# Optimization experiments

Hardware: AMD Instinct MI355X
Metric: run time of the kernel (lower is better)

The kernel has to match this reference:

```python
import jax, jax.numpy as jnp
import numpy as np

B, S, D, NL, H, KV, F, V, R = 4, 1024, 2048, 2, 16, 4, 8192, 32000, 16
HD = D // H                      # 128, Llama-3 head dim
LORA_SCALE = 32.0 / 16.0         # alpha / r
ROPE_THETA = 500000.0
EPS = 1e-5


def _rope_tables(seq_len, hd):
    inv = 1.0 / (ROPE_THETA ** (jnp.arange(0, hd, 2, dtype=jnp.float32) / hd))
    freqs = jnp.arange(seq_len, dtype=jnp.float32)[:, None] * inv[None, :]   # [S, hd/2]
    emb = jnp.concatenate([freqs, freqs], axis=-1)                           # [S, hd]
    return jnp.cos(emb), jnp.sin(emb)


def _apply_rope(x, cos, sin):
    # x: [B, S, nh, HD]; LLaMA rotate_half convention
    h = x.shape[-1] // 2
    rot = jnp.concatenate([-x[..., h:], x[..., :h]], axis=-1)
    return x * cos[None, :, None, :] + rot * sin[None, :, None, :]


def _rmsnorm(x, w):
    return x * jax.lax.rsqrt(jnp.mean(x * x, axis=-1, keepdims=True) + EPS) * w


def _forward(embed, wq, wk, wv, wo, laq, lbq, lav, lbv, wg, wu, wd, n1, n2, nf,
             input_ids, attention_mask):
    b, s = input_ids.shape
    cos, sin = _rope_tables(s, HD)
    amask = attention_mask.astype(bool)
    # causal AND key-padding mask: [B, 1, S, S]
    mask = jnp.tril(jnp.ones((s, s), bool))[None, None] & amask[:, None, None, :]
    x = embed[input_ids]                                   # [B, S, D]
    for l in range(NL):
        h = _rmsnorm(x, n1[l])
        # base projection + LoRA adapter (q and v only, as in target_modules)
        q = h @ wq[l] + ((h @ laq[l].T) @ lbq[l].T) * LORA_SCALE
        k = h @ wk[l]
        v = h @ wv[l] + ((h @ lav[l].T) @ lbv[l].T) * LORA_SCALE
        q = _apply_rope(q.reshape(b, s, H, HD), cos, sin)
        k = _apply_rope(k.reshape(b, s, KV, HD), cos, sin)
        v = v.reshape(b, s, KV, HD)
        k = jnp.repeat(k, H // KV, axis=2)                 # GQA expand
        v = jnp.repeat(v, H // KV, axis=2)
        scores = jnp.einsum('bqhd,bkhd->bhqk', q, k) / jnp.float32(np.sqrt(HD))
        scores = jnp.where(mask, scores, jnp.float32(-1e9))
        attn = jax.nn.softmax(scores, axis=-1)
        o = jnp.einsum('bhqk,bkhd->bqhd', attn, v).reshape(b, s, D)
        x = x + o @ wo[l]
        h2 = _rmsnorm(x, n2[l])
        x = x + (jax.nn.silu(h2 @ wg[l]) * (h2 @ wu[l])) @ wd[l]
    h = _rmsnorm(x, nf)                                    # final norm -> last_hidden_state
    m = attention_mask.astype(jnp.float32)[..., None]
    return (h * m).sum(axis=1) / jnp.clip(m.sum(axis=1), 1e-9)   # masked mean pool [B, D]


def setup_inputs() -> dict:
    key = jax.random.key(0)
    ks = jax.random.split(key, 14)
    sd = 0.02
    nrm = lambda k, shape: sd * jax.random.normal(k, shape, dtype=jnp.float32)
    return {
        'embed': nrm(ks[0], (V, D)),
        'wq': nrm(ks[1], (NL, D, D)),
        'wk': nrm(ks[2], (NL, D, KV * HD)),
        'wv': nrm(ks[3], (NL, D, KV * HD)),
        'wo': nrm(ks[4], (NL, D, D)),
        'laq': nrm(ks[5], (NL, R, D)),
        'lbq': nrm(ks[6], (NL, D, R)),
        'lav': nrm(ks[7], (NL, R, D)),
        'lbv': nrm(ks[8], (NL, KV * HD, R)),
        'wg': nrm(ks[9], (NL, D, F)),
        'wu': nrm(ks[10], (NL, D, F)),
        'wd': nrm(ks[11], (NL, F, D)),
        'n1': jnp.ones((NL, D), jnp.float32),
        'n2': jnp.ones((NL, D), jnp.float32),
        'nf': jnp.ones((D,), jnp.float32),
        'input_ids': jax.random.randint(ks[12], (B, S), 0, V, dtype=jnp.int32),
        'attention_mask': jnp.ones((B, S), jnp.int32),
    }


def reference(embed, wq, wk, wv, wo, laq, lbq, lav, lbv, wg, wu, wd, n1, n2, nf,
              input_ids, attention_mask):
    return _forward(embed, wq, wk, wv, wo, laq, lbq, lav, lbv, wg, wu, wd,
                    n1, n2, nf, input_ids, attention_mask)
```

## Files before the change

kernel.cpp:

```cpp
#include <hip/hip_runtime.h>
#include <math.h>

#define B_  4
#define S_  1024
#define D_  2048
#define NL_ 2
#define H_  16
#define KV_ 4
#define F_  8192
#define R_  16
#define HD_ 128
#define BS_ (B_*S_)
#define QT2 32
#define KBLK 64
#define NQKV 3072

typedef unsigned short u16;
typedef __attribute__((ext_vector_type(8))) __bf16 bf16x8;
typedef __attribute__((ext_vector_type(4))) float  f32x4;

__device__ __forceinline__ u16 f2bf(float f) {
    unsigned x = __float_as_uint(f);
    unsigned r = (x + 0x7fffu + ((x >> 16) & 1u)) >> 16;
    return (u16)r;
}
__device__ __forceinline__ float bf2f(u16 u) {
    return __uint_as_float(((unsigned)u) << 16);
}

__device__ __forceinline__ void gload16(const void* g, void* l) {
    __builtin_amdgcn_global_load_lds((const __attribute__((address_space(1))) void*)g,
                                     (__attribute__((address_space(3))) void*)l, 16, 0, 0);
}

__global__ void embed_kernel(const float* __restrict__ embed,
                             const int* __restrict__ ids,
                             float* __restrict__ x) {
    int tok = blockIdx.x;
    int id  = ids[tok];
    const float4* src = (const float4*)(embed + (size_t)id * D_);
    float4*       dst = (float4*)(x + (size_t)tok * D_);
    for (int i = threadIdx.x; i < D_/4; i += blockDim.x) dst[i] = src[i];
}

template<int OUTBF>
__global__ __launch_bounds__(256) void rmsnorm_kernel(const float* __restrict__ x,
                                                      const float* __restrict__ w,
                                                      void* __restrict__ out) {
    int row = blockIdx.x;
    const float4* xr = (const float4*)(x + (size_t)row * D_);
    float ss = 0.f;
    for (int i = threadIdx.x; i < D_/4; i += 256) {
        float4 v = xr[i];
        ss += v.x*v.x + v.y*v.y + v.z*v.z + v.w*v.w;
    }
    __shared__ float red[4];
    for (int off = 32; off; off >>= 1) ss += __shfl_down(ss, off);
    if ((threadIdx.x & 63) == 0) red[threadIdx.x >> 6] = ss;
    __syncthreads();
    float tot = red[0] + red[1] + red[2] + red[3];
    float scale = rsqrtf(tot / (float)D_ + 1e-5f);
    const float4* w4 = (const float4*)w;
    for (int i = threadIdx.x; i < D_/4; i += 256) {
        float4 v = xr[i], g = w4[i];
        float a = v.x*scale*g.x, b = v.y*scale*g.y, c = v.z*scale*g.z, d = v.w*scale*g.w;
        if (OUTBF) {
            ushort4 o; o.x = f2bf(a); o.y = f2bf(b); o.z = f2bf(c); o.w = f2bf(d);
            ((ushort4*)((u16*)out + (size_t)row * D_))[i] = o;
        } else {
            float4 o; o.x = a; o.y = b; o.z = c; o.w = d;
            ((float4*)((float*)out + (size_t)row * D_))[i] = o;
        }
    }
}

__global__ __launch_bounds__(256) void convt_kernel(const float* __restrict__ in,
                                                    u16* __restrict__ outT,
                                                    int K, int N) {
    __shared__ float tile[64][65];
    int k0 = blockIdx.y * 64, n0 = blockIdx.x * 64;
    int t = threadIdx.x, r = t >> 4, c4 = (t & 15) * 4;
    #pragma unroll
    for (int p = 0; p < 4; p++) {
        float4 v = *(const float4*)(in + (size_t)(k0 + p * 16 + r) * N + n0 + c4);
        tile[p*16+r][c4]   = v.x; tile[p*16+r][c4+1] = v.y;
        tile[p*16+r][c4+2] = v.z; tile[p*16+r][c4+3] = v.w;
    }
    __syncthreads();
    #pragma unroll
    for (int p = 0; p < 4; p++) {
        int n = p * 16 + r;
        ushort4 o;
        o.x = f2bf(tile[c4][n]);   o.y = f2bf(tile[c4+1][n]);
        o.z = f2bf(tile[c4+2][n]); o.w = f2bf(tile[c4+3][n]);
        *(ushort4*)(outT + (size_t)(n0 + n) * K + k0 + c4) = o;
    }
}

__global__ __launch_bounds__(256) void convt_qkv(const float* __restrict__ wq,
                                                 const float* __restrict__ wk,
                                                 const float* __restrict__ wv,
                                                 u16* __restrict__ outT) {
    int z = blockIdx.z;
    int N = (z == 0) ? 2048 : 512;
    if (blockIdx.x * 64 >= N) return;
    const float* in = (z == 0) ? wq : (z == 1 ? wk : wv);
    u16* out = outT + (z == 0 ? 0 : (z == 1 ? (size_t)2048 * D_ : (size_t)2560 * D_));
    __shared__ float tile[64][65];
    int k0 = blockIdx.y * 64, n0 = blockIdx.x * 64;
    int t = threadIdx.x, r = t >> 4, c4 = (t & 15) * 4;
    #pragma unroll
    for (int p = 0; p < 4; p++) {
        float4 v = *(const float4*)(in + (size_t)(k0 + p * 16 + r) * N + n0 + c4);
        tile[p*16+r][c4]   = v.x; tile[p*16+r][c4+1] = v.y;
        tile[p*16+r][c4+2] = v.z; tile[p*16+r][c4+3] = v.w;
    }
    __syncthreads();
    #pragma unroll
    for (int p = 0; p < 4; p++) {
        int n = p * 16 + r;
        ushort4 o;
        o.x = f2bf(tile[c4][n]);   o.y = f2bf(tile[c4+1][n]);
        o.z = f2bf(tile[c4+2][n]); o.w = f2bf(tile[c4+3][n]);
        *(ushort4*)(out + (size_t)(n0 + n) * D_ + k0 + c4) = o;
    }
}

__global__ __launch_bounds__(256) void convt_gu2(const float* __restrict__ G,
                                                 const float* __restrict__ U,
                                                 u16* __restrict__ outT) {
    __shared__ float tile[64][65];
    int k0 = blockIdx.y * 64, n0 = blockIdx.x * 64;
    int t = threadIdx.x, r = t >> 4, c4 = (t & 15) * 4;
    #pragma unroll
    for (int slot = 0; slot < 2; slot++) {
        const float* in = slot ? U : G;
        if (slot) __syncthreads();
        #pragma unroll
        for (int p = 0; p < 4; p++) {
            float4 v = *(const float4*)(in + (size_t)(k0 + p * 16 + r) * F_ + n0 + c4);
            tile[p*16+r][c4]   = v.x; tile[p*16+r][c4+1] = v.y;
            tile[p*16+r][c4+2] = v.z; tile[p*16+r][c4+3] = v.w;
        }
        __syncthreads();
        #pragma unroll
        for (int p = 0; p < 4; p++) {
            int n = p * 16 + r;
            int orow = n0 + n;
            int wrow = ((orow >> 7) << 8) + slot * 128 + (orow & 127);
            ushort4 o;
            o.x = f2bf(tile[c4][n]);   o.y = f2bf(tile[c4+1][n]);
            o.z = f2bf(tile[c4+2][n]); o.w = f2bf(tile[c4+3][n]);
            *(ushort4*)(outT + (size_t)wrow * D_ + k0 + c4) = o;
        }
    }
}

template<int ACC>
__global__ __launch_bounds__(256) void gemm_bt(const u16* __restrict__ A,
                                               const u16* __restrict__ Bt,
                                               float* __restrict__ C,
                                               int N, int K) {
    __shared__ __align__(16) u16 As[128*64];
    __shared__ __align__(16) u16 Bs[128*64];
    int tid = threadIdx.x, lane = tid & 63;
    int wid = tid >> 6, wm = wid >> 1, wn = wid & 1;
    int m0 = blockIdx.y * 128, n0 = blockIdx.x * 128;
    const u16* Ab = A  + (size_t)m0 * K;
    const u16* Bb = Bt + (size_t)n0 * K;
    f32x4 acc[4][4] = {};
    for (int k0 = 0; k0 < K; k0 += 64) {
        #pragma unroll
        for (int qq = 0; qq < 4; qq++) {
            int u = qq * 256 + tid;
            int row = u >> 3, cu = u & 7, scu = cu ^ (row & 7);
            size_t goff = (size_t)row * K + k0 + scu * 8;
            gload16(Ab + goff, (char*)As + u * 16);
            gload16(Bb + goff, (char*)Bs + u * 16);
        }
        __syncthreads();
        #pragma unroll
        for (int kk = 0; kk < 2; kk++) {
            int cu = kk * 4 + (lane >> 4);
            bf16x8 af[4], bfr[4];
            #pragma unroll
            for (int i = 0; i < 4; i++) {
                int ar = wm * 64 + i * 16 + (lane & 15);
                af[i]  = *(const bf16x8*)((const char*)As + (((ar << 3) | (cu ^ (ar & 7))) << 4));
                int br = wn * 64 + i * 16 + (lane & 15);
                bfr[i] = *(const bf16x8*)((const char*)Bs + (((br << 3) | (cu ^ (br & 7))) << 4));
            }
            #pragma unroll
            for (int i = 0; i < 4; i++)
                #pragma unroll
                for (int j = 0; j < 4; j++)
                    acc[i][j] = __builtin_amdgcn_mfma_f32_16x16x32_bf16(af[i], bfr[j], acc[i][j], 0, 0, 0);
        }
        __syncthreads();
    }
    int r0 = (lane >> 4) * 4, c0 = lane & 15;
    #pragma unroll
    for (int i = 0; i < 4; i++)
        #pragma unroll
        for (int j = 0; j < 4; j++) {
            int row = m0 + wm * 64 + i * 16 + r0;
            int col = n0 + wn * 64 + j * 16 + c0;
            float* cp = C + (size_t)row * N + col;
            #pragma unroll
            for (int r = 0; r < 4; r++) {
                if (ACC) cp[(size_t)r * N] += acc[i][j][r];
                else     cp[(size_t)r * N] = acc[i][j][r];
            }
        }
}

__global__ __launch_bounds__(512) void gemm_gateup8(const u16* __restrict__ A,
                                                    const u16* __restrict__ Wt,
                                                    u16* __restrict__ act,
                                                    int Nact, int K) {
    __shared__ __align__(16) u16 ring[2][4][8192];
    int tid = threadIdx.x, lane = tid & 63;
    int w = tid >> 6;
    int wm = w >> 2, wn = w & 3;
    int g = lane >> 4, li = lane & 15;
    int m0 = blockIdx.y * 256, n0 = blockIdx.x * 256;
    const u16* Ab = A  + (size_t)m0 * K;
    const u16* Bb = Wt + (size_t)n0 * K;
    int nt = K >> 6;

    f32x4 acc[8][4] = {};

    #define STG(s, t_, kh, P)                                                        \
        do {                                                                         \
            int u_ = (P) * 512 + tid;                                                \
            int j_ = u_ >> 3, cc_ = u_ & 7;                                          \
            int sc_ = cc_ ^ (j_ & 7);                                                \
            int row_ = 2 * j_ + (sc_ >> 2);                                          \
            int kc_ = (t_) * 64 + (kh) * 32 + (sc_ & 3) * 8;                         \
            gload16(Ab + (size_t)row_ * K + kc_, (char*)&ring[0][s][0] + u_ * 16);   \
            gload16(Bb + (size_t)row_ * K + kc_, (char*)&ring[1][s][0] + u_ * 16);   \
        } while (0)

    #define FRAG(op, s, r) (*(const bf16x8*)((const char*)&ring[op][s][0] +          \
        (((((r) >> 1) << 3) | (((((r) & 1) << 2) | g) ^ (((r) >> 1) & 7))) << 4)))

    STG(0, 0, 0, 0); STG(0, 0, 0, 1);
    STG(1, 0, 1, 0); STG(1, 0, 1, 1);
    STG(2, 1, 0, 0); STG(2, 1, 0, 1);

    for (int t = 0; t < nt; t++) {
        int s0  = (2 * t) & 3;
        int s1  = (2 * t + 1) & 3;
        int sW0 = (2 * t + 3) & 3;
        int sW1 = s0;
        bf16x8 af[4], bfr[4];

        if (t == nt - 1) asm volatile("s_waitcnt vmcnt(4)" ::: "memory");
        else             asm volatile("s_waitcnt vmcnt(8)" ::: "memory");
        __builtin_amdgcn_s_barrier();
        __builtin_amdgcn_sched_barrier(0);
        #pragma unroll
        for (int j = 0; j < 4; j++) bfr[j] = FRAG(1, s0, wn * 64 + j * 16 + li);
        #pragma unroll
        for (int i = 0; i < 4; i++) af[i] = FRAG(0, s0, wm * 128 + i * 16 + li);
        if (t + 1 < nt) STG(sW0, t + 1, 1, 0);
        asm volatile("s_waitcnt lgkmcnt(0)" ::: "memory");
        __builtin_amdgcn_sched_barrier(0);
        __builtin_amdgcn_s_setprio(1);
        #pragma unroll
        for (int i = 0; i < 4; i++)
            #pragma unroll
            for (int j = 0; j < 4; j++)
                acc[i][j] = __builtin_amdgcn_mfma_f32_16x16x32_bf16(af[i], bfr[j], acc[i][j], 0, 0, 0);
        __builtin_amdgcn_s_setprio(0);

        __builtin_amdgcn_s_barrier();
        __builtin_amdgcn_sched_barrier(0);
        #pragma unroll
        for (int i = 0; i < 4; i++) af[i] = FRAG(0, s0, wm * 128 + 64 + i * 16 + li);
        if (t + 1 < nt) STG(sW0, t + 1, 1, 1);
        asm volatile("s_waitcnt lgkmcnt(0)" ::: "memory");
        __builtin_amdgcn_sched_barrier(0);
        __builtin_amdgcn_s_setprio(1);
        #pragma unroll
        for (int i = 0; i < 4; i++)
            #pragma unroll
            for (int j = 0; j < 4; j++)
                acc[4 + i][j] = __builtin_amdgcn_mfma_f32_16x16x32_bf16(af[i], bfr[j], acc[4 + i][j], 0, 0, 0);
        __builtin_amdgcn_s_setprio(0);

        if (t == nt - 1) asm volatile("s_waitcnt vmcnt(0)" ::: "memory");
        else             asm volatile("s_waitcnt vmcnt(8)" ::: "memory");
        __builtin_amdgcn_s_barrier();
        __builtin_amdgcn_sched_barrier(0);
        #pragma unroll
        for (int j = 0; j < 4; j++) bfr[j] = FRAG(1, s1, wn * 64 + j * 16 + li);
        #pragma unroll
        for (int i = 0; i < 4; i++) af[i] = FRAG(0, s1, wm * 128 + i * 16 + li);
        if (t + 2 < nt) STG(sW1, t + 2, 0, 0);
        asm volatile("s_waitcnt lgkmcnt(0)" ::: "memory");
        __builtin_amdgcn_sched_barrier(0);
        __builtin_amdgcn_s_setprio(1);
        #pragma unroll
        for (int i = 0; i < 4; i++)
            #pragma unroll
            for (int j = 0; j < 4; j++)
                acc[i][j] = __builtin_amdgcn_mfma_f32_16x16x32_bf16(af[i], bfr[j], acc[i][j], 0, 0, 0);
        __builtin_amdgcn_s_setprio(0);

        __builtin_amdgcn_s_barrier();
        __builtin_amdgcn_sched_barrier(0);
        #pragma unroll
        for (int i = 0; i < 4; i++) af[i] = FRAG(0, s1, wm * 128 + 64 + i * 16 + li);
        if (t + 2 < nt) STG(sW1, t + 2, 0, 1);
        asm volatile("s_waitcnt lgkmcnt(0)" ::: "memory");
        __builtin_amdgcn_sched_barrier(0);
        __builtin_amdgcn_s_setprio(1);
        #pragma unroll
        for (int i = 0; i < 4; i++)
            #pragma unroll
            for (int j = 0; j < 4; j++)
                acc[4 + i][j] = __builtin_amdgcn_mfma_f32_16x16x32_bf16(af[i], bfr[j], acc[4 + i][j], 0, 0, 0);
        __builtin_amdgcn_s_setprio(0);
    }
    #undef STG
    #undef FRAG

    __syncthreads();
    float* X = (float*)&ring[0][0][0];
    if (wn >= 2) {
        float* Rr = X + (size_t)(wm * 2 + (wn - 2)) * 8192;
        #pragma unroll
        for (int i = 0; i < 8; i++)
            #pragma unroll
            for (int j = 0; j < 4; j++)
                #pragma unroll
                for (int r = 0; r < 4; r++) {
                    int row = i * 16 + g * 4 + r;
                    int col = j * 16 + li;
                    Rr[row * 64 + (col ^ (((row >> 2) & 3) << 4))] = acc[i][j][r];
                }
    }
    __syncthreads();
    if (wn < 2) {
        const float* Rr = X + (size_t)(wm * 2 + wn) * 8192;
        int colbase = (n0 >> 1) + wn * 64;
        #pragma unroll
        for (int i = 0; i < 8; i++)
            #pragma unroll
            for (int j = 0; j < 4; j++)
                #pragma unroll
                for (int r = 0; r < 4; r++) {
                    int row = i * 16 + g * 4 + r;
                    int col = j * 16 + li;
                    float gv = acc[i][j][r];
                    float uv = Rr[row * 64 + (col ^ (((row >> 2) & 3) << 4))];
                    float s = gv / (1.f + __expf(-gv));
                    act[(size_t)(m0 + wm * 128 + row) * Nact + colbase + col] = f2bf(s * uv);
                }
    }
}

__global__ __launch_bounds__(256) void lora_a2(const u16* __restrict__ h,
                                               const float* __restrict__ laq,
                                               const float* __restrict__ lav,
                                               float* __restrict__ t16q,
                                               float* __restrict__ t16v) {
    const float* la = blockIdx.y ? lav : laq;
    float* t16 = blockIdx.y ? t16v : t16q;
    int r = threadIdx.x >> 4;
    int c = threadIdx.x & 15;
    int row = blockIdx.x * 16 + r;
    const ushort4* hr = (const ushort4*)(h + (size_t)row * D_);
    const float4* lr = (const float4*)(la + (size_t)c * D_);
    float acc = 0.f;
    #pragma unroll 4
    for (int i = 0; i < D_/4; i++) {
        ushort4 a = hr[i]; float4 b = lr[i];
        acc += bf2f(a.x)*b.x + bf2f(a.y)*b.y + bf2f(a.z)*b.z + bf2f(a.w)*b.w;
    }
    t16[(size_t)row * R_ + c] = acc;
}

__global__ __launch_bounds__(256) void lora_b2(const float* __restrict__ t16q,
                                               const float* __restrict__ t16v,
                                               const float* __restrict__ lbq,
                                               const float* __restrict__ lbv,
                                               float* __restrict__ qkv) {
    int isv = blockIdx.y;
    const float* t16 = isv ? t16v : t16q;
    const float* lb  = isv ? lbv : lbq;
    int N = isv ? (KV_*HD_) : D_;
    float* out = qkv + (size_t)blockIdx.x * NQKV + (isv ? 2560 : 0);
    int row = blockIdx.x;
    __shared__ float ts[R_];
    if (threadIdx.x < R_) ts[threadIdx.x] = t16[(size_t)row * R_ + threadIdx.x];
    __syncthreads();
    for (int d = threadIdx.x; d < N; d += 256) {
        const float4* lbr = (const float4*)(lb + (size_t)d * R_);
        float acc = 0.f;
        #pragma unroll
        for (int r4 = 0; r4 < 4; r4++) {
            float4 v = lbr[r4];
            acc += v.x*ts[r4*4] + v.y*ts[r4*4+1] + v.z*ts[r4*4+2] + v.w*ts[r4*4+3];
        }
        out[d] += 2.0f * acc;
    }
}

__global__ void qkconv_rope(const float* __restrict__ qkv,
                            u16* __restrict__ Qc, u16* __restrict__ Kc) {
    int tok = blockIdx.x, hh = blockIdx.y, t = threadIdx.x;
    int b = tok >> 10, s = tok & (S_ - 1);
    float inv = __expf(-(float)t * (13.122363377404328f / 64.0f));
    float f = (float)s * inv;
    float c = __cosf(f), si = __sinf(f);
    const float* src;
    u16* dst;
    if (hh < H_) {
        src = qkv + (size_t)tok * NQKV + hh * HD_;
        dst = Qc + (((size_t)(b * H_ + hh)) * S_ + s) * HD_;
    } else {
        int kh = hh - H_;
        src = qkv + (size_t)tok * NQKV + 2048 + kh * HD_;
        dst = Kc + (((size_t)(b * KV_ + kh)) * S_ + s) * HD_;
    }
    float x0 = src[t], x1 = src[t + 64];
    dst[t]      = f2bf(x0 * c - x1 * si);
    dst[t + 64] = f2bf(x1 * c + x0 * si);
}

__global__ __launch_bounds__(256) void vconv_t(const float* __restrict__ qkv,
                                               u16* __restrict__ Vt) {
    __shared__ float tile[32][33];
    int s0 = blockIdx.x * 32, d0 = blockIdx.y * 32;
    int bk = blockIdx.z;
    int b = bk >> 2, kvh = bk & 3;
    int t = threadIdx.x;
    int r = t >> 3, c4 = (t & 7) * 4;
    float4 v = *(const float4*)(qkv + (size_t)(b * S_ + s0 + r) * NQKV + 2560 + kvh * HD_ + d0 + c4);
    tile[r][c4] = v.x; tile[r][c4+1] = v.y; tile[r][c4+2] = v.z; tile[r][c4+3] = v.w;
    __syncthreads();
    int dr = t >> 3, s4 = (t & 7) * 4;
    ushort4 o;
    o.x = f2bf(tile[s4][dr]);   o.y = f2bf(tile[s4+1][dr]);
    o.z = f2bf(tile[s4+2][dr]); o.w = f2bf(tile[s4+3][dr]);
    *(ushort4*)(Vt + (((size_t)(b * KV_ + kvh)) * HD_ + d0 + dr) * S_ + s0 + s4) = o;
}

__global__ __launch_bounds__(512) void flash_attn(const u16* __restrict__ Qc,
                                                  const u16* __restrict__ Kc,
                                                  const u16* __restrict__ Vt,
                                                  const int* __restrict__ am,
                                                  u16* __restrict__ o) {
    __shared__ __align__(16) u16 Ks[64 * 128];
    __shared__ __align__(16) u16 Vs[128 * 64];
    __shared__ __align__(16) u16 Ps[8][16][72];
    __shared__ int am_s[KBLK];
    int qt = gridDim.x - 1 - blockIdx.x;
    int kvh = blockIdx.y, b = blockIdx.z;
    int tid = threadIdx.x, lane = tid & 63, w = tid >> 6;
    int g = lane >> 4, li = lane & 15;
    int h = kvh * 4 + (w & 3);
    int qrow0 = qt * QT2 + (w >> 2) * 16;

    bf16x8 qf[4];
    const u16* qb = Qc + (((size_t)(b * H_ + h)) * S_ + qrow0 + li) * HD_;
    #pragma unroll
    for (int dd = 0; dd < 4; dd++) qf[dd] = *(const bf16x8*)(qb + dd * 32 + g * 8);

    float m_r[4], l_r[4];
    f32x4 oacc[8];
    #pragma unroll
    for (int r = 0; r < 4; r++) { m_r[r] = -1e30f; l_r[r] = 0.f; }
    #pragma unroll
    for (int d = 0; d < 8; d++) oacc[d] = (f32x4){0.f, 0.f, 0.f, 0.f};

    const u16* Kg = Kc + ((size_t)(b * KV_ + kvh)) * S_ * HD_;
    const u16* Vg = Vt + ((size_t)(b * KV_ + kvh)) * HD_ * S_;
    int qg0 = qrow0 + g * 4;
    int nkv = (qt * QT2 + QT2 - 1) >> 6;

    for (int kvt = 0; kvt <= nkv; kvt++) {
        int kv0 = kvt * KBLK;
        #pragma unroll
        for (int qq = 0; qq < 2; qq++) {
            int u = qq * 512 + tid;
            int krow = u >> 4, p = u & 15;
            gload16(Kg + (size_t)(kv0 + krow) * HD_ + (p ^ (krow & 7)) * 8, (char*)Ks + u * 16);
            int vrow = u >> 3, pv = u & 7;
            gload16(Vg + (size_t)vrow * S_ + kv0 + (pv ^ (vrow & 7)) * 8, (char*)Vs + u * 16);
        }
        if (tid < KBLK) am_s[tid] = am[b * S_ + kv0 + tid];
        __syncthreads();

        if (kv0 <= qrow0 + 15) {
            float ps[4][4];
            #pragma unroll
            for (int kt = 0; kt < 4; kt++) {
                f32x4 sa = (f32x4){0.f, 0.f, 0.f, 0.f};
                int row = kt * 16 + li;
                #pragma unroll
                for (int dd = 0; dd < 4; dd++) {
                    int c = dd * 4 + g;
                    bf16x8 kf = *(const bf16x8*)((const char*)Ks + ((row * 16 + (c ^ (row & 7))) << 4));
                    sa = __builtin_amdgcn_mfma_f32_16x16x32_bf16(qf[dd], kf, sa, 0, 0, 0);
                }
                int kcol = kv0 + kt * 16 + li;
                int amok = am_s[kt * 16 + li];
                #pragma unroll
                for (int r = 0; r < 4; r++) {
                    float s = sa[r] * 0.08838834764831845f;
                    ps[kt][r] = (amok && kcol <= qg0 + r) ? s : -1e9f;
                }
            }

            float rmax[4], rsum[4], scl[4];
            #pragma unroll
            for (int r = 0; r < 4; r++)
                rmax[r] = fmaxf(fmaxf(ps[0][r], ps[1][r]), fmaxf(ps[2][r], ps[3][r]));
            #pragma unroll
            for (int msk = 1; msk < 16; msk <<= 1)
                #pragma unroll
                for (int r = 0; r < 4; r++) rmax[r] = fmaxf(rmax[r], __shfl_xor(rmax[r], msk));
            #pragma unroll
            for (int r = 0; r < 4; r++) {
                float mn = fmaxf(m_r[r], rmax[r]);
                scl[r] = __expf(m_r[r] - mn);
                m_r[r] = mn;
                rsum[r] = 0.f;
            }
            #pragma unroll
            for (int kt = 0; kt < 4; kt++)
                #pragma unroll
                for (int r = 0; r < 4; r++) {
                    float p = __expf(ps[kt][r] - m_r[r]);
                    ps[kt][r] = p;
                    rsum[r] += p;
                }
            #pragma unroll
            for (int msk = 1; msk < 16; msk <<= 1)
                #pragma unroll
                for (int r = 0; r < 4; r++) rsum[r] += __shfl_xor(rsum[r], msk);
            #pragma unroll
            for (int r = 0; r < 4; r++) l_r[r] = l_r[r] * scl[r] + rsum[r];
            #pragma unroll
            for (int d = 0; d < 8; d++)
                #pragma unroll
                for (int r = 0; r < 4; r++) oacc[d][r] *= scl[r];

            #pragma unroll
            for (int kt = 0; kt < 4; kt++)
                #pragma unroll
                for (int r = 0; r < 4; r++)
                    Ps[w][g * 4 + r][kt * 16 + li] = f2bf(ps[kt][r]);
            bf16x8 pf[2];
            #pragma unroll
            for (int ks = 0; ks < 2; ks++)
                pf[ks] = *(const bf16x8*)&Ps[w][li][ks * 32 + g * 8];

            #pragma unroll
            for (int dblk = 0; dblk < 8; dblk++) {
                int row = dblk * 16 + li;
                #pragma unroll
                for (int ks = 0; ks < 2; ks++) {
                    int c = ks * 4 + g;
                    bf16x8 vf = *(const bf16x8*)((const char*)Vs + ((row * 8 + (c ^ (row & 7))) << 4));
                    oacc[dblk] = __builtin_amdgcn_mfma_f32_16x16x32_bf16(pf[ks], vf, oacc[dblk], 0, 0, 0);
                }
            }
        }
        __syncthreads();
    }

    float invl[4];
    #pragma unroll
    for (int r = 0; r < 4; r++) invl[r] = 1.f / l_r[r];
    #pragma unroll
    for (int dblk = 0; dblk < 8; dblk++)
        #pragma unroll
        for (int r = 0; r < 4; r++) {
            int qrow = qg0 + r;
            o[(((size_t)b * S_ + qrow) * H_ + h) * HD_ + dblk * 16 + li] =
                f2bf(oacc[dblk][r] * invl[r]);
        }
}

__global__ __launch_bounds__(256) void pool_kernel(const float* __restrict__ h,
                                                   const int* __restrict__ am,
                                                   float* __restrict__ out) {
    int b = blockIdx.y;
    int d = blockIdx.x * 256 + threadIdx.x;
    float acc = 0.f, ms = 0.f;
    for (int s = 0; s < S_; s++) {
        float mm = (float)am[b * S_ + s];
        ms  += mm;
        acc += mm * h[((size_t)b * S_ + s) * D_ + d];
    }
    out[(size_t)b * D_ + d] = acc / fmaxf(ms, 1e-9f);
}

extern "C" void kernel_launch(void* const* d_in, const int* in_sizes, int n_in,
                              void* d_out, int out_size, void* d_ws, size_t ws_size,
                              hipStream_t stream) {
    const float* embed = (const float*)d_in[0];
    const float* wq    = (const float*)d_in[1];
    const float* wk    = (const float*)d_in[2];
    const float* wv    = (const float*)d_in[3];
    const float* wo    = (const float*)d_in[4];
    const float* laq   = (const float*)d_in[5];
    const float* lbq   = (const float*)d_in[6];
    const float* lav   = (const float*)d_in[7];
    const float* lbv   = (const float*)d_in[8];
    const float* wg    = (const float*)d_in[9];
    const float* wu    = (const float*)d_in[10];
    const float* wd    = (const float*)d_in[11];
    const float* n1    = (const float*)d_in[12];
    const float* n2    = (const float*)d_in[13];
    const float* nf    = (const float*)d_in[14];
    const int*   ids   = (const int*)d_in[15];
    const int*   am    = (const int*)d_in[16];
    float* out = (float*)d_out;

    char* base = (char*)d_ws;
    float* x    = (float*)base;
    u16*   hbf  = (u16*)(base + 33554432);
    u16*   obf  = (u16*)(base + 50331648);
    char*  Rg   = base + 67108864;
    float* qkv  = (float*)Rg;
    float* t16v = (float*)(base + 117440512);
    u16*   act  = (u16*)Rg;
    float* hf   = (float*)Rg;
    float* t16q = (float*)(base + 134217728);
    u16*   wT0  = (u16*)(base + 134479872);
    u16*   Qc   = (u16*)(base + 201588736);
    u16*   Kc   = (u16*)(base + 218365952);
    u16*   Vtb  = (u16*)(base + 222560256);

    embed_kernel<<<BS_, 256, 0, stream>>>(embed, ids, x);

    for (int l = 0; l < NL_; l++) {
        const float* wql = wq + (size_t)l * D_ * D_;
        const float* wkl = wk + (size_t)l * D_ * (KV_*HD_);
        const float* wvl = wv + (size_t)l * D_ * (KV_*HD_);
        const float* wol = wo + (size_t)l * D_ * D_;
        const float* wgl = wg + (size_t)l * D_ * F_;
        const float* wul = wu + (size_t)l * D_ * F_;
        const float* wdl = wd + (size_t)l * F_ * D_;

        rmsnorm_kernel<1><<<BS_, 256, 0, stream>>>(x, n1 + (size_t)l * D_, hbf);

        convt_qkv<<<dim3(32, 32, 3), 256, 0, stream>>>(wql, wkl, wvl, wT0);
        gemm_bt<0><<<dim3(NQKV/128, BS_/128), 256, 0, stream>>>(hbf, wT0, qkv, NQKV, D_);

        lora_a2<<<dim3(BS_/16, 2), 256, 0, stream>>>(hbf, laq + (size_t)l * R_ * D_,
                                                     lav + (size_t)l * R_ * D_, t16q, t16v);
        lora_b2<<<dim3(BS_, 2), 256, 0, stream>>>(t16q, t16v,
                                                  lbq + (size_t)l * D_ * R_,
                                                  lbv + (size_t)l * (KV_*HD_) * R_, qkv);

        qkconv_rope<<<dim3(BS_, H_ + KV_), 64, 0, stream>>>(qkv, Qc, Kc);
        vconv_t<<<dim3(S_/32, HD_/32, B_*KV_), 256, 0, stream>>>(qkv, Vtb);

        flash_attn<<<dim3(S_/QT2, KV_, B_), 512, 0, stream>>>(Qc, Kc, Vtb, am, obf);

        convt_kernel<<<dim3(D_/64, D_/64), 256, 0, stream>>>(wol, wT0, D_, D_);
        gemm_bt<1><<<dim3(D_/128, BS_/128), 256, 0, stream>>>(obf, wT0, x, D_, D_);

        rmsnorm_kernel<1><<<BS_, 256, 0, stream>>>(x, n2 + (size_t)l * D_, hbf);
        convt_gu2<<<dim3(F_/64, D_/64), 256, 0, stream>>>(wgl, wul, wT0);
        gemm_gateup8<<<dim3((2*F_)/256, BS_/256), 512, 0, stream>>>(hbf, wT0, act, F_, D_);
        convt_kernel<<<dim3(D_/64, F_/64), 256, 0, stream>>>(wdl, wT0, F_, D_);
        gemm_bt<1><<<dim3(D_/128, BS_/128), 256, 0, stream>>>(act, wT0, x, D_, F_);
    }

    rmsnorm_kernel<0><<<BS_, 256, 0, stream>>>(x, nf, hf);
    pool_kernel<<<dim3(D_/256, B_), 256, 0, stream>>>(hf, am, out);
}
```

Before: 1.962 ms.

## Fuse LoRA-B into RoPE/V conversion, merge wo transpose, add ring-buffered down GEMM

After: 1.902 ms. 1.03x faster.

```diff
diff --git a/kernel.cpp b/kernel.cpp
--- a/kernel.cpp
+++ b/kernel.cpp
@@ -100,12 +100,14 @@
 __global__ __launch_bounds__(256) void convt_qkv(const float* __restrict__ wq,
                                                  const float* __restrict__ wk,
                                                  const float* __restrict__ wv,
+                                                 const float* __restrict__ wo,
                                                  u16* __restrict__ outT) {
     int z = blockIdx.z;
-    int N = (z == 0) ? 2048 : 512;
+    int N = (z == 0 || z == 3) ? 2048 : 512;
     if (blockIdx.x * 64 >= N) return;
-    const float* in = (z == 0) ? wq : (z == 1 ? wk : wv);
-    u16* out = outT + (z == 0 ? 0 : (z == 1 ? (size_t)2048 * D_ : (size_t)2560 * D_));
+    const float* in = (z == 0) ? wq : (z == 1 ? wk : (z == 2 ? wv : wo));
+    size_t roff = (z == 0) ? 0 : (z == 1 ? 2048 : (z == 2 ? 2560 : 3072));
+    u16* out = outT + roff * D_;
     __shared__ float tile[64][65];
     int k0 = blockIdx.y * 64, n0 = blockIdx.x * 64;
     int t = threadIdx.x, r = t >> 4, c4 = (t & 15) * 4;
@@ -359,6 +361,115 @@
                     act[(size_t)(m0 + wm * 128 + row) * Nact + colbase + col] = f2bf(s * uv);
                 }
     }
+}
+
+__global__ __launch_bounds__(512) void gemm_down_ring(const u16* __restrict__ A,
+                                                      const u16* __restrict__ Bt,
+                                                      float* __restrict__ C,
+                                                      int N, int K) {
+    __shared__ __align__(16) u16 ringA[4][8192];
+    __shared__ __align__(16) u16 ringB[4][4096];
+    int tid = threadIdx.x, lane = tid & 63;
+    int w = tid >> 6;
+    int wm = w >> 1, wn = w & 1;
+    int g = lane >> 4, li = lane & 15;
+    int m0 = blockIdx.y * 256, n0 = blockIdx.x * 128;
+    const u16* Ab = A  + (size_t)m0 * K;
+    const u16* Bb = Bt + (size_t)n0 * K;
+    int nt = K >> 6;
+
+    f32x4 acc[4][4] = {};
+
+    #define STGA(s, t_, kh, P)                                                       \
+        do {                                                                         \
+            int u_ = (P) * 512 + tid;                                                \
+            int j_ = u_ >> 3, cc_ = u_ & 7;                                          \
+            int sc_ = cc_ ^ (j_ & 7);                                                \
+            int row_ = 2 * j_ + (sc_ >> 2);                                          \
+            int kc_ = (t_) * 64 + (kh) * 32 + (sc_ & 3) * 8;                         \
+            gload16(Ab + (size_t)row_ * K + kc_, (char*)&ringA[s][0] + u_ * 16);     \
+        } while (0)
+    #define STGB(s, t_, kh)                                                          \
+        do {                                                                         \
+            int u_ = tid;                                                            \
+            int j_ = u_ >> 3, cc_ = u_ & 7;                                          \
+            int sc_ = cc_ ^ (j_ & 7);                                                \
+            int row_ = 2 * j_ + (sc_ >> 2);                                          \
+            int kc_ = (t_) * 64 + (kh) * 32 + (sc_ & 3) * 8;                         \
+            gload16(Bb + (size_t)row_ * K + kc_, (char*)&ringB[s][0] + u_ * 16);     \
+        } while (0)
+
+    #define FRAGA(s, r) (*(const bf16x8*)((const char*)&ringA[s][0] +                \
+        (((((r) >> 1) << 3) | (((((r) & 1) << 2) | g) ^ (((r) >> 1) & 7))) << 4)))
+    #define FRAGB(s, r) (*(const bf16x8*)((const char*)&ringB[s][0] +                \
+        (((((r) >> 1) << 3) | (((((r) & 1) << 2) | g) ^ (((r) >> 1) & 7))) << 4)))
+
+    STGA(0, 0, 0, 0); STGA(0, 0, 0, 1); STGB(0, 0, 0);
+    STGA(1, 0, 1, 0); STGA(1, 0, 1, 1); STGB(1, 0, 1);
+    STGA(2, 1, 0, 0); STGA(2, 1, 0, 1); STGB(2, 1, 0);
+
+    for (int t = 0; t < nt; t++) {
+        int s0  = (2 * t) & 3;
+        int s1  = (2 * t + 1) & 3;
+        int sW0 = (2 * t + 3) & 3;
+        int sW1 = s0;
+        bf16x8 af[4], bfr[4];
+
+        if (t == nt - 1) asm volatile("s_waitcnt vmcnt(3)" ::: "memory");
+        else             asm volatile("s_waitcnt vmcnt(6)" ::: "memory");
+        __builtin_amdgcn_s_barrier();
+        __builtin_amdgcn_sched_barrier(0);
+        #pragma unroll
+        for (int j = 0; j < 4; j++) bfr[j] = FRAGB(s0, wn * 64 + j * 16 + li);
+        #pragma unroll
+        for (int i = 0; i < 4; i++) af[i] = FRAGA(s0, wm * 64 + i * 16 + li);
+        if (t + 1 < nt) { STGA(sW0, t + 1, 1, 0); STGA(sW0, t + 1, 1, 1); STGB(sW0, t + 1, 1); }
+        asm volatile("s_waitcnt lgkmcnt(0)" ::: "memory");
+        __builtin_amdgcn_sched_barrier(0);
+        __builtin_amdgcn_s_setprio(1);
+        #pragma unroll
+        for (int i = 0; i < 4; i++)
+            #pragma unroll
+            for (int j = 0; j < 4; j++)
+                acc[i][j] = __builtin_amdgcn_mfma_f32_16x16x32_bf16(af[i], bfr[j], acc[i][j], 0, 0, 0);
+        __builtin_amdgcn_s_setprio(0);
+
+        if (t == nt - 1) asm volatile("s_waitcnt vmcnt(0)" ::: "memory");
+        else             asm volatile("s_waitcnt vmcnt(6)" ::: "memory");
+        __builtin_amdgcn_s_barrier();
+        __builtin_amdgcn_sched_barrier(0);
+        #pragma unroll
+        for (int j = 0; j < 4; j++) bfr[j] = FRAGB(s1, wn * 64 + j * 16 + li);
+        #pragma unroll
+        for (int i = 0; i < 4; i++) af[i] = FRAGA(s1, wm * 64 + i * 16 + li);
+        if (t + 2 < nt) { STGA(sW1, t + 2, 0, 0); STGA(sW1, t + 2, 0, 1); STGB(sW1, t + 2, 0); }
+        asm volatile("s_waitcnt lgkmcnt(0)" ::: "memory");
+        __builtin_amdgcn_sched_barrier(0);
+        __builtin_amdgcn_s_setprio(1);
+        #pragma unroll
+        for (int i = 0; i < 4; i++)
+            #pragma unroll
+            for (int j = 0; j < 4; j++)
+                acc[i][j] = __builtin_amdgcn_mfma_f32_16x16x32_bf16(af[i], bfr[j], acc[i][j], 0, 0, 0);
+        __builtin_amdgcn_s_setprio(0);
+    }
+    #undef STGA
+    #undef STGB
+    #undef FRAGA
+    #undef FRAGB
+
+    int r0 = g * 4, c0 = li;
+    #pragma unroll
+    for (int i = 0; i < 4; i++)
+        #pragma unroll
+        for (int j = 0; j < 4; j++) {
+            int row = m0 + wm * 64 + i * 16 + r0;
+            int col = n0 + wn * 64 + j * 16 + c0;
+            float* cp = C + (size_t)row * N + col;
+            #pragma unroll
+            for (int r = 0; r < 4; r++)
+                cp[(size_t)r * N] += acc[i][j][r];
+        }
 }
 
 __global__ __launch_bounds__(256) void lora_a2(const u16* __restrict__ h,
@@ -382,64 +493,78 @@
     t16[(size_t)row * R_ + c] = acc;
 }
 
-__global__ __launch_bounds__(256) void lora_b2(const float* __restrict__ t16q,
-                                               const float* __restrict__ t16v,
-                                               const float* __restrict__ lbq,
-                                               const float* __restrict__ lbv,
-                                               float* __restrict__ qkv) {
-    int isv = blockIdx.y;
-    const float* t16 = isv ? t16v : t16q;
-    const float* lb  = isv ? lbv : lbq;
-    int N = isv ? (KV_*HD_) : D_;
-    float* out = qkv + (size_t)blockIdx.x * NQKV + (isv ? 2560 : 0);
-    int row = blockIdx.x;
-    __shared__ float ts[R_];
-    if (threadIdx.x < R_) ts[threadIdx.x] = t16[(size_t)row * R_ + threadIdx.x];
-    __syncthreads();
-    for (int d = threadIdx.x; d < N; d += 256) {
-        const float4* lbr = (const float4*)(lb + (size_t)d * R_);
-        float acc = 0.f;
-        #pragma unroll
-        for (int r4 = 0; r4 < 4; r4++) {
-            float4 v = lbr[r4];
-            acc += v.x*ts[r4*4] + v.y*ts[r4*4+1] + v.z*ts[r4*4+2] + v.w*ts[r4*4+3];
-        }
-        out[d] += 2.0f * acc;
-    }
-}
-
 __global__ void qkconv_rope(const float* __restrict__ qkv,
+                            const float* __restrict__ t16q,
+                            const float* __restrict__ lbq,
                             u16* __restrict__ Qc, u16* __restrict__ Kc) {
     int tok = blockIdx.x, hh = blockIdx.y, t = threadIdx.x;
     int b = tok >> 10, s = tok & (S_ - 1);
+    __shared__ float ts[R_];
+    if (t < R_) ts[t] = t16q[(size_t)tok * R_ + t];
+    __syncthreads();
     float inv = __expf(-(float)t * (13.122363377404328f / 64.0f));
     float f = (float)s * inv;
     float c = __cosf(f), si = __sinf(f);
-    const float* src;
+    float x0, x1;
     u16* dst;
     if (hh < H_) {
-        src = qkv + (size_t)tok * NQKV + hh * HD_;
+        const float* src = qkv + (size_t)tok * NQKV + hh * HD_;
+        int d0 = hh * HD_ + t;
+        float l0 = 0.f, l1 = 0.f;
+        const float4* b0 = (const float4*)(lbq + (size_t)d0 * R_);
+        const float4* b1 = (const float4*)(lbq + (size_t)(d0 + 64) * R_);
+        #pragma unroll
+        for (int r4 = 0; r4 < 4; r4++) {
+            float4 v0 = b0[r4], v1 = b1[r4];
+            l0 += v0.x*ts[r4*4] + v0.y*ts[r4*4+1] + v0.z*ts[r4*4+2] + v0.w*ts[r4*4+3];
+            l1 += v1.x*ts[r4*4] + v1.y*ts[r4*4+1] + v1.z*ts[r4*4+2] + v1.w*ts[r4*4+3];
+        }
+        x0 = src[t] + 2.0f * l0;
+        x1 = src[t + 64] + 2.0f * l1;
         dst = Qc + (((size_t)(b * H_ + hh)) * S_ + s) * HD_;
     } else {
         int kh = hh - H_;
-        src = qkv + (size_t)tok * NQKV + 2048 + kh * HD_;
+        const float* src = qkv + (size_t)tok * NQKV + 2048 + kh * HD_;
+        x0 = src[t];
+        x1 = src[t + 64];
         dst = Kc + (((size_t)(b * KV_ + kh)) * S_ + s) * HD_;
     }
-    float x0 = src[t], x1 = src[t + 64];
     dst[t]      = f2bf(x0 * c - x1 * si);
     dst[t + 64] = f2bf(x1 * c + x0 * si);
 }
 
 __global__ __launch_bounds__(256) void vconv_t(const float* __restrict__ qkv,
+                                               const float* __restrict__ t16v,
+                                               const float* __restrict__ lbv,
                                                u16* __restrict__ Vt) {
     __shared__ float tile[32][33];
+    __shared__ float ts[32][16];
     int s0 = blockIdx.x * 32, d0 = blockIdx.y * 32;
     int bk = blockIdx.z;
     int b = bk >> 2, kvh = bk & 3;
     int t = threadIdx.x;
+    #pragma unroll
+    for (int p = 0; p < 2; p++) {
+        int idx = p * 256 + t;
+        ts[idx >> 4][idx & 15] = t16v[(size_t)(b * S_ + s0 + (idx >> 4)) * R_ + (idx & 15)];
+    }
     int r = t >> 3, c4 = (t & 7) * 4;
     float4 v = *(const float4*)(qkv + (size_t)(b * S_ + s0 + r) * NQKV + 2560 + kvh * HD_ + d0 + c4);
-    tile[r][c4] = v.x; tile[r][c4+1] = v.y; tile[r][c4+2] = v.z; tile[r][c4+3] = v.w;
+    __syncthreads();
+    float vv[4] = {v.x, v.y, v.z, v.w};
+    #pragma unroll
+    for (int e = 0; e < 4; e++) {
+        int d = kvh * HD_ + d0 + c4 + e;
+        const float4* lr = (const float4*)(lbv + (size_t)d * R_);
+        float l = 0.f;
+        #pragma unroll
+        for (int r4 = 0; r4 < 4; r4++) {
+            float4 w = lr[r4];
+            l += w.x*ts[r][r4*4] + w.y*ts[r][r4*4+1] + w.z*ts[r][r4*4+2] + w.w*ts[r][r4*4+3];
+        }
+        vv[e] += 2.0f * l;
+    }
+    tile[r][c4] = vv[0]; tile[r][c4+1] = vv[1]; tile[r][c4+2] = vv[2]; tile[r][c4+3] = vv[3];
     __syncthreads();
     int dr = t >> 3, s4 = (t & 7) * 4;
     ushort4 o;
@@ -650,28 +775,26 @@
 
         rmsnorm_kernel<1><<<BS_, 256, 0, stream>>>(x, n1 + (size_t)l * D_, hbf);
 
-        convt_qkv<<<dim3(32, 32, 3), 256, 0, stream>>>(wql, wkl, wvl, wT0);
+        convt_qkv<<<dim3(32, 32, 4), 256, 0, stream>>>(wql, wkl, wvl, wol, wT0);
         gemm_bt<0><<<dim3(NQKV/128, BS_/128), 256, 0, stream>>>(hbf, wT0, qkv, NQKV, D_);
 
         lora_a2<<<dim3(BS_/16, 2), 256, 0, stream>>>(hbf, laq + (size_t)l * R_ * D_,
                                                      lav + (size_t)l * R_ * D_, t16q, t16v);
-        lora_b2<<<dim3(BS_, 2), 256, 0, stream>>>(t16q, t16v,
-                                                  lbq + (size_t)l * D_ * R_,
-                                                  lbv + (size_t)l * (KV_*HD_) * R_, qkv);
-
-        qkconv_rope<<<dim3(BS_, H_ + KV_), 64, 0, stream>>>(qkv, Qc, Kc);
-        vconv_t<<<dim3(S_/32, HD_/32, B_*KV_), 256, 0, stream>>>(qkv, Vtb);
+
+        qkconv_rope<<<dim3(BS_, H_ + KV_), 64, 0, stream>>>(qkv, t16q,
+                                                            lbq + (size_t)l * D_ * R_, Qc, Kc);
+        vconv_t<<<dim3(S_/32, HD_/32, B_*KV_), 256, 0, stream>>>(qkv, t16v,
+                                                                 lbv + (size_t)l * (KV_*HD_) * R_, Vtb);
 
         flash_attn<<<dim3(S_/QT2, KV_, B_), 512, 0, stream>>>(Qc, Kc, Vtb, am, obf);
 
-        convt_kernel<<<dim3(D_/64, D_/64), 256, 0, stream>>>(wol, wT0, D_, D_);
-        gemm_bt<1><<<dim3(D_/128, BS_/128), 256, 0, stream>>>(obf, wT0, x, D_, D_);
+        gemm_bt<1><<<dim3(D_/128, BS_/128), 256, 0, stream>>>(obf, wT0 + (size_t)3072 * D_, x, D_, D_);
 
         rmsnorm_kernel<1><<<BS_, 256, 0, stream>>>(x, n2 + (size_t)l * D_, hbf);
         convt_gu2<<<dim3(F_/64, D_/64), 256, 0, stream>>>(wgl, wul, wT0);
         gemm_gateup8<<<dim3((2*F_)/256, BS_/256), 512, 0, stream>>>(hbf, wT0, act, F_, D_);
         convt_kernel<<<dim3(D_/64, F_/64), 256, 0, stream>>>(wdl, wT0, F_, D_);
-        gemm_bt<1><<<dim3(D_/128, BS_/128), 256, 0, stream>>>(act, wT0, x, D_, F_);
+        gemm_down_ring<<<dim3(D_/128, BS_/256), 512, 0, stream>>>(act, wT0, x, D_, F_);
     }
 
     rmsnorm_kernel<0><<<BS_, 256, 0, stream>>>(x, nf, hf);
```
